# Kernel tuning notes

Measured on AMD Instinct MI355X. Metric: run time of the kernel, lower is better.

## Reference

```python
import jax, jax.numpy as jnp
import numpy as np

SIZE = 5           # kernel size and num_rbfs
MUL = 16           # multiplicity of 0e and 1o in irreps_in/out
CROP = SIZE // 2
# e3nn FullyConnectedTensorProduct path weights (normalization='component', path_normalization='element'):
# path_weight = sqrt((2*l_out+1) / fan_in), fan_in = sum over paths into that output of mul1*mul2.
# out 0e: paths (0e,0e)+(1o,1o) -> fan_in=32; out 1o: paths (0e,1o)+(1o,0e) -> fan_in=32.
PW0 = (1.0 / 32.0) ** 0.5          # scalar output paths
PW1 = (3.0 / 32.0) ** 0.5          # vector output paths
INV_SQRT3 = 3.0 ** -0.5            # wigner-3j values: w3j(1,0,1)=w3j(0,1,1)=w3j(1,1,0)=delta/sqrt(3)


def _lattice_consts():
    # lattice of kernel offsets, steps=(1,1,1) keeps all SIZE points per axis
    r = jnp.linspace(-1.0, 1.0, SIZE)
    lat = jnp.stack(jnp.meshgrid(r, r, r, indexing='ij'), axis=-1)   # [5,5,5,3]
    d = jnp.linalg.norm(lat, axis=-1)                                # [5,5,5]
    # soft_one_hot_linspace(basis='smooth_finite', endpoint=True) over [0,1] with SIZE bins
    values = jnp.linspace(0.0, 1.0, SIZE)
    step = values[1] - values[0]
    diff = (d[..., None] - values) / step                            # [5,5,5,5]
    def sus(t):  # soft unit step: exp(-1/t) for t>0 else 0
        return jnp.where(t > 0, jnp.exp(-1.0 / jnp.where(t > 0, t, 1.0)), 0.0)
    emb = 1.14136 * np.float32(np.e ** 2) * sus(diff + 1.0) * sus(1.0 - diff)
    # spherical harmonics lmax=1, normalize=True, 'component' normalization
    n = lat / jnp.maximum(d, 1e-12)[..., None]                       # zero vector -> 0 (like F.normalize)
    sh0 = jnp.ones_like(d)                                           # l=0 component-normalized
    sh1 = (3.0 ** 0.5) * n                                           # l=1 component-normalized, [5,5,5,3]
    return emb, sh0, sh1


def _make_kernel(weight):
    """emb @ weight -> per-voxel TP weights; tp.right(sh, w) -> [5,5,5,in=64,out=64] kernel."""
    emb, sh0, sh1 = _lattice_consts()
    w = emb @ weight                                                 # [5,5,5,1024]
    S = w.shape[:3]
    blk = MUL * MUL
    # path order: (0e,0e->0e), (0e,1o->1o), (1o,0e->1o), (1o,1o->0e)
    w1, w2, w3, w4 = [w[..., i * blk:(i + 1) * blk].reshape(*S, MUL, MUL) for i in range(4)]
    k_ss = PW0 * w1 * sh0[..., None, None]                           # [s,u,w]   scalar in -> scalar out
    k_sv = PW1 * INV_SQRT3 * jnp.einsum('...uw,...k->...uwk', w2, sh1)   # [s,u,w,k] scalar in -> vector out
    k_vs = PW0 * INV_SQRT3 * jnp.einsum('...uw,...i->...uiw', w4, sh1)   # [s,u,i,w] vector in -> scalar out
    eye3 = jnp.eye(3, dtype=w.dtype)
    k_vv = PW1 * INV_SQRT3 * (w3 * sh0[..., None, None])[..., :, None, :, None] \
           * eye3[None, None, None, None, :, None, :]                # [s,u,i,w,k] vector in -> vector out
    top = jnp.concatenate([k_ss, k_sv.reshape(*S, MUL, 3 * MUL)], axis=-1)            # [s,16,64]
    bot = jnp.concatenate([k_vs.reshape(*S, 3 * MUL, MUL),
                           k_vv.reshape(*S, 3 * MUL, 3 * MUL)], axis=-1)              # [s,48,64]
    kernel = jnp.concatenate([top, bot], axis=-2)                    # [5,5,5,in,out]
    return jnp.transpose(kernel, (4, 3, 0, 1, 2))                    # 'xyzio->oixyz'


def reference(x, weight, w_sc0, w_sc1):
    B = x.shape[0]
    sp = x.shape[2:]
    # self-connection: e3nn Linear (per-irrep mixing, 1/sqrt(fan_in) norm), then crop
    xs = x[:, :MUL]                                                  # scalars [B,16,X,Y,Z]
    xv = x[:, MUL:].reshape(B, MUL, 3, *sp)                          # vectors [B,16,3,X,Y,Z]
    inv = 1.0 / MUL ** 0.5
    sc_s = jnp.einsum('buxyz,uw->bwxyz', xs, w_sc0) * inv
    sc_v = (jnp.einsum('buixyz,uw->bwixyz', xv, w_sc1) * inv).reshape(B, 3 * MUL, *sp)
    sc = jnp.concatenate([sc_s, sc_v], axis=1)[:, :, CROP:-CROP, CROP:-CROP, CROP:-CROP]
    # equivariant kernel + dense conv3d (torch conv3d = correlation = VALID conv here)
    kernel = _make_kernel(weight)                                    # [64,64,5,5,5]
    conv = jax.lax.conv_general_dilated(x, kernel, (1, 1, 1), 'VALID',
                                        dimension_numbers=('NCDHW', 'OIDHW', 'NCDHW'))
    return sc + conv


def setup_inputs() -> dict:
    key = jax.random.key(0)
    k1, k2, k3, k4 = jax.random.split(key, 4)
    weight_numel = 4 * MUL * MUL  # 1024
    return {
        'x': jax.random.normal(k1, (1, 4 * MUL, 56, 56, 56), dtype=jnp.float32),
        'weight': jax.random.normal(k2, (SIZE, weight_numel), dtype=jnp.float32)
                  * np.float32((2.0 / weight_numel) ** 0.5),  # kaiming_normal(relu)
        'w_sc0': jax.random.normal(k3, (MUL, MUL), dtype=jnp.float32),
        'w_sc1': jax.random.normal(k4, (MUL, MUL), dtype=jnp.float32),
    }
```

## Files before the change

kernel.cpp:

```cpp
#include <hip/hip_runtime.h>
#include <hip/hip_bf16.h>

typedef unsigned short ush;
typedef __bf16 v8bf __attribute__((ext_vector_type(8)));
typedef float f32x4 __attribute__((ext_vector_type(4)));
typedef float f32x16 __attribute__((ext_vector_type(16)));

#define SPD 56
#define OSD 52
#define SP3 175616
#define N_A_ELEMS (2*125*64*32)
#define NCX 5488
#define NBA 2008

__global__ void aux_kernel(const float* __restrict__ x, ush* __restrict__ xb,
                           const float* __restrict__ weight, const float* __restrict__ w_sc0,
                           const float* __restrict__ w_sc1, ush* __restrict__ A) {
    __shared__ float t[64 * 33];
    const int bid = blockIdx.x;
    const int tid = threadIdx.x;
    if (bid < NCX) {
        const int s0 = (bid % 2744) * 64;
        const int cg = bid / 2744;
        const int w = tid >> 6, l = tid & 63;
        #pragma unroll
        for (int k = 0; k < 8; k++) {
            int c = w * 8 + k;
            t[l * 33 + c] = x[(cg * 32 + c) * SP3 + s0 + l];
        }
        __syncthreads();
        int v = tid >> 2, qq = tid & 3;
        union { ush u[8]; uint4 q4; } pk;
        #pragma unroll
        for (int j = 0; j < 8; j++) {
            __hip_bfloat16 b = __float2bfloat16(t[v * 33 + qq * 8 + j]);
            pk.u[j] = *(ush*)&b;
        }
        *(uint4*)(xb + ((size_t)(cg * SP3 + s0 + v)) * 32 + qq * 8) = pk.q4;
        return;
    }
    int f = (bid - NCX) * 256 + tid;
    if (f >= N_A_ELEMS) {
        if (f < N_A_ELEMS + 2048) A[f] = 0;
        return;
    }
    int c   = f & 31;
    int o   = (f >> 5) & 63;
    int t2  = f >> 11;
    int tau = t2 % 125;
    int cg  = t2 / 125;
    int i   = cg * 32 + c;
    int dz = tau / 25, dy = (tau / 5) % 5, dx = tau % 5;
    float rz = -1.f + 0.5f * dz, ry = -1.f + 0.5f * dy, rx = -1.f + 0.5f * dx;
    float d = sqrtf(rz * rz + ry * ry + rx * rx);
    float dm = fmaxf(d, 1e-12f);
    float nv[3] = { rz / dm, ry / dm, rx / dm };
    float emb[5];
    #pragma unroll
    for (int m = 0; m < 5; m++) {
        float diff = 4.f * d - (float)m;
        float ta = diff + 1.f, tb = 1.f - diff;
        float sa = ta > 0.f ? expf(-1.f / ta) : 0.f;
        float sb = tb > 0.f ? expf(-1.f / tb) : 0.f;
        emb[m] = 1.14136f * 7.3890560989306495f * sa * sb;
    }
    const float PW0 = 0.17677669529663687f;
    const float PW1 = 0.30618621784789724f;
    const float IS3 = 0.57735026918962576f;
    float val = 0.f;
    int widx = -1; float scale = 0.f;
    if (i < 16) {
        if (o < 16) { widx = i * 16 + o;                         scale = PW0; }
        else        { int wc = (o - 16) / 3, kc = (o - 16) % 3;
                      widx = 256 + i * 16 + wc;                  scale = PW1 * nv[kc]; }
    } else {
        int u = (i - 16) / 3, ic = (i - 16) % 3;
        if (o < 16) { widx = 768 + u * 16 + o;                   scale = PW0 * nv[ic]; }
        else        { int wc = (o - 16) / 3, jc = (o - 16) % 3;
                      if (ic == jc) { widx = 512 + u * 16 + wc;  scale = PW1 * IS3; } }
    }
    if (widx >= 0) {
        float wv = 0.f;
        #pragma unroll
        for (int m = 0; m < 5; m++) wv += emb[m] * weight[m * 1024 + widx];
        val = scale * wv;
    }
    if (tau == 62) {
        if (i < 16 && o < 16) val += 0.25f * w_sc0[i * 16 + o];
        else if (i >= 16 && o >= 16) {
            int u = (i - 16) / 3, ic = (i - 16) % 3;
            int wc = (o - 16) / 3, jc = (o - 16) % 3;
            if (ic == jc) val += 0.25f * w_sc1[u * 16 + wc];
        }
    }
    __hip_bfloat16 b = __float2bfloat16(val);
    A[f] = *(ush*)&b;
}

__launch_bounds__(256, 2)
__global__ void conv_main(const ush* __restrict__ A, const ush* __restrict__ xb,
                          float* __restrict__ out) {
    __shared__ ush patch[32768];

    const int b  = blockIdx.x;
    const int bp = (b & 7) * 148 + (b >> 3);
    if (bp >= 1183) return;
    const int bx = bp % 13;
    const int t1 = bp / 13;
    const int by = t1 % 13;
    const int bz = t1 / 13;
    const int x0 = bx * 4, y0 = by * 4;
    const int z0 = (bz == 6) ? 44 : bz * 8;

    const int tid  = threadIdx.x;
    const int wv   = tid >> 6;
    const int lane = tid & 63;
    const int lhi  = lane >> 5;
    const int rbase32 = ((lane >> 4) & 1) * 64 + ((lane >> 2) & 3) * 8 + (lane & 3);
    const ush* Aw = A + (lane & 31) * 32 + lhi * 8;

    f32x16 acc[2][4];
    #pragma unroll
    for (int mt = 0; mt < 2; mt++)
        #pragma unroll
        for (int nt = 0; nt < 4; nt++)
            acc[mt][nt] = (f32x16)(0.f);

    for (int cg = 0; cg < 2; cg++) {
        __syncthreads();
        #pragma unroll 4
        for (int it = 0; it < 12; it++) {
            int u   = tid + it * 256;
            int qq  = u & 3;
            int vox = u >> 2;
            int xp = vox & 7, yp = (vox >> 3) & 7, zp = vox >> 6;
            const ush* g = xb + ((size_t)((cg * SPD + z0 + zp) * SPD + (y0 + yp)) * SPD + (x0 + xp)) * 32 + qq * 8;
            uint4 v = *(const uint4*)g;
            int slot = vox * 4 + ((qq + vox + (vox >> 3)) & 3);
            *(uint4*)(patch + slot * 8) = v;
        }
        __syncthreads();

        const int t0 = wv * 32;
        int dz = t0 / 25; int rr = t0 - dz * 25; int dy = rr / 5; int dx = rr - dy * 5;

        #pragma unroll 2
        for (int j = 0; j < 32; j++) {
            int t = t0 + j;
            int vb = dz * 64 + dy * 8 + dx;
            if (vb > 292) vb = 0;
            int v0 = vb + rbase32;
            int pre = v0 + (v0 >> 3);
            int slot0 = v0 * 4 + ((lhi + pre) & 3);
            int slot1 = v0 * 4 + ((2 + lhi + pre) & 3);

            v8bf bf[4][2];
            #pragma unroll
            for (int nt = 0; nt < 4; nt++) {
                bf[nt][0] = *(const v8bf*)(patch + slot0 * 8 + nt * 4096);
                bf[nt][1] = *(const v8bf*)(patch + slot1 * 8 + nt * 4096);
            }

            int toff = (t < 125) ? (cg * 125 + t) : 250;
            v8bf af[2][2];
            #pragma unroll
            for (int mt = 0; mt < 2; mt++)
                #pragma unroll
                for (int h = 0; h < 2; h++)
                    af[mt][h] = *(const v8bf*)(Aw + (size_t)toff * 2048 + mt * 1024 + h * 16);

            #pragma unroll
            for (int h = 0; h < 2; h++)
                #pragma unroll
                for (int mt = 0; mt < 2; mt++)
                    #pragma unroll
                    for (int nt = 0; nt < 4; nt++)
                        acc[mt][nt] = __builtin_amdgcn_mfma_f32_32x32x16_bf16(af[mt][h], bf[nt][h], acc[mt][nt], 0, 0, 0);

            int c1 = (dx == 4);
            dx = c1 ? 0 : dx + 1;
            int c2 = c1 & (dy == 4);
            dy = c2 ? 0 : dy + c1;
            dz += c2;
        }
    }

    __syncthreads();
    float* red = (float*)patch;
    if (wv >= 2) {
        #pragma unroll
        for (int mt = 0; mt < 2; mt++)
            #pragma unroll
            for (int nt = 0; nt < 4; nt++) {
                float* p = red + (wv - 2) * 8192 + (mt * 4 + nt) * 1024 + lane * 16;
                #pragma unroll
                for (int s = 0; s < 4; s++) {
                    f32x4 v = { acc[mt][nt][s*4+0], acc[mt][nt][s*4+1], acc[mt][nt][s*4+2], acc[mt][nt][s*4+3] };
                    *(f32x4*)(p + s * 4) = v;
                }
            }
    }
    __syncthreads();
    if (wv < 2) {
        #pragma unroll
        for (int mt = 0; mt < 2; mt++)
            #pragma unroll
            for (int nt = 0; nt < 4; nt++) {
                float* p = red + wv * 8192 + (mt * 4 + nt) * 1024 + lane * 16;
                #pragma unroll
                for (int s = 0; s < 4; s++) {
                    f32x4 v = *(const f32x4*)(p + s * 4);
                    f32x4 m = { acc[mt][nt][s*4+0], acc[mt][nt][s*4+1], acc[mt][nt][s*4+2], acc[mt][nt][s*4+3] };
                    *(f32x4*)(p + s * 4) = v + m;
                }
            }
    }
    __syncthreads();

    const int yy = y0 + ((lane >> 2) & 3);
    const int xx = x0 + (lane & 3);
    #pragma unroll
    for (int k = 0; k < 2; k++) {
        int fi = wv * 2 + k;
        int mt = fi >> 2, nt = fi & 3;
        int zz = z0 + nt * 2 + ((lane >> 4) & 1);
        #pragma unroll
        for (int s = 0; s < 4; s++) {
            f32x4 v = *(const f32x4*)(red + fi * 1024 + lane * 16 + s * 4);
            v += *(const f32x4*)(red + 8192 + fi * 1024 + lane * 16 + s * 4);
            #pragma unroll
            for (int e = 0; e < 4; e++) {
                int o = mt * 32 + e + 8 * s + 4 * lhi;
                out[((o * OSD + zz) * OSD + yy) * OSD + xx] = v[e];
            }
        }
    }
}

extern "C" void kernel_launch(void* const* d_in, const int* in_sizes, int n_in,
                              void* d_out, int out_size, void* d_ws, size_t ws_size,
                              hipStream_t stream) {
    const float* x      = (const float*)d_in[0];
    const float* weight = (const float*)d_in[1];
    const float* w_sc0  = (const float*)d_in[2];
    const float* w_sc1  = (const float*)d_in[3];
    float* out = (float*)d_out;

    ush* A  = (ush*)d_ws;
    ush* xb = (ush*)((char*)d_ws + (2 << 20));

    aux_kernel<<<NCX + NBA, 256, 0, stream>>>(x, xb, weight, w_sc0, w_sc1, A);
    conv_main<<<1184, 256, 0, stream>>>(A, xb, out);
}
```

Before: 231.7 us.

## Split conv waves into 2 N-groups by 2 K-groups and raise occupancy

Each block's four waves are reorganized from four tap-range K-splits into two output-column groups times two tap-range groups. This halves the per-wave accumulator tiles and B-fragment LDS reads, allowing launch bounds of 3 blocks per CU and a smaller shared patch buffer. The cross-wave reduction now uses one exchange and stores output directly, removing a barrier and a pass through LDS. In exchange, each wave loads A fragments for twice as many taps, doubling global/L2 traffic for the weight matrix.

```diff
diff --git a/kernel.cpp b/kernel.cpp
--- a/kernel.cpp
+++ b/kernel.cpp
@@ -97,10 +97,10 @@
     A[f] = *(ush*)&b;
 }
 
-__launch_bounds__(256, 2)
+__launch_bounds__(256, 3)
 __global__ void conv_main(const ush* __restrict__ A, const ush* __restrict__ xb,
                           float* __restrict__ out) {
-    __shared__ ush patch[32768];
+    __shared__ ush patch[24576];
 
     const int b  = blockIdx.x;
     const int bp = (b & 7) * 148 + (b >> 3);
@@ -114,16 +114,18 @@
 
     const int tid  = threadIdx.x;
     const int wv   = tid >> 6;
+    const int ns   = wv & 1;
+    const int ks   = wv >> 1;
     const int lane = tid & 63;
     const int lhi  = lane >> 5;
     const int rbase32 = ((lane >> 4) & 1) * 64 + ((lane >> 2) & 3) * 8 + (lane & 3);
     const ush* Aw = A + (lane & 31) * 32 + lhi * 8;
 
-    f32x16 acc[2][4];
+    f32x16 acc[2][2];
     #pragma unroll
     for (int mt = 0; mt < 2; mt++)
         #pragma unroll
-        for (int nt = 0; nt < 4; nt++)
+        for (int nt = 0; nt < 2; nt++)
             acc[mt][nt] = (f32x16)(0.f);
 
     for (int cg = 0; cg < 2; cg++) {
@@ -141,11 +143,11 @@
         }
         __syncthreads();
 
-        const int t0 = wv * 32;
+        const int t0 = ks * 64;
         int dz = t0 / 25; int rr = t0 - dz * 25; int dy = rr / 5; int dx = rr - dy * 5;
 
         #pragma unroll 2
-        for (int j = 0; j < 32; j++) {
+        for (int j = 0; j < 64; j++) {
             int t = t0 + j;
             int vb = dz * 64 + dy * 8 + dx;
             if (vb > 292) vb = 0;
@@ -154,11 +156,12 @@
             int slot0 = v0 * 4 + ((lhi + pre) & 3);
             int slot1 = v0 * 4 + ((2 + lhi + pre) & 3);
 
-            v8bf bf[4][2];
-            #pragma unroll
-            for (int nt = 0; nt < 4; nt++) {
-                bf[nt][0] = *(const v8bf*)(patch + slot0 * 8 + nt * 4096);
-                bf[nt][1] = *(const v8bf*)(patch + slot1 * 8 + nt * 4096);
+            v8bf bf[2][2];
+            #pragma unroll
+            for (int nt = 0; nt < 2; nt++) {
+                int off = (ns * 2 + nt) * 4096;
+                bf[nt][0] = *(const v8bf*)(patch + slot0 * 8 + off);
+                bf[nt][1] = *(const v8bf*)(patch + slot1 * 8 + off);
             }
 
             int toff = (t < 125) ? (cg * 125 + t) : 250;
@@ -174,7 +177,7 @@
                 #pragma unroll
                 for (int mt = 0; mt < 2; mt++)
                     #pragma unroll
-                    for (int nt = 0; nt < 4; nt++)
+                    for (int nt = 0; nt < 2; nt++)
                         acc[mt][nt] = __builtin_amdgcn_mfma_f32_32x32x16_bf16(af[mt][h], bf[nt][h], acc[mt][nt], 0, 0, 0);
 
             int c1 = (dx == 4);
@@ -187,12 +190,12 @@
 
     __syncthreads();
     float* red = (float*)patch;
-    if (wv >= 2) {
+    if (ks == 1) {
         #pragma unroll
         for (int mt = 0; mt < 2; mt++)
             #pragma unroll
-            for (int nt = 0; nt < 4; nt++) {
-                float* p = red + (wv - 2) * 8192 + (mt * 4 + nt) * 1024 + lane * 16;
+            for (int nt = 0; nt < 2; nt++) {
+                float* p = red + ns * 4096 + (mt * 2 + nt) * 1024 + lane * 16;
                 #pragma unroll
                 for (int s = 0; s < 4; s++) {
                     f32x4 v = { acc[mt][nt][s*4+0], acc[mt][nt][s*4+1], acc[mt][nt][s*4+2], acc[mt][nt][s*4+3] };
@@ -201,39 +204,27 @@
             }
     }
     __syncthreads();
-    if (wv < 2) {
+    if (ks == 0) {
+        const int yy = y0 + ((lane >> 2) & 3);
+        const int xx = x0 + (lane & 3);
         #pragma unroll
         for (int mt = 0; mt < 2; mt++)
             #pragma unroll
-            for (int nt = 0; nt < 4; nt++) {
-                float* p = red + wv * 8192 + (mt * 4 + nt) * 1024 + lane * 16;
+            for (int nt = 0; nt < 2; nt++) {
+                const float* p = red + ns * 4096 + (mt * 2 + nt) * 1024 + lane * 16;
+                int zz = z0 + (ns * 2 + nt) * 2 + ((lane >> 4) & 1);
                 #pragma unroll
                 for (int s = 0; s < 4; s++) {
                     f32x4 v = *(const f32x4*)(p + s * 4);
                     f32x4 m = { acc[mt][nt][s*4+0], acc[mt][nt][s*4+1], acc[mt][nt][s*4+2], acc[mt][nt][s*4+3] };
-                    *(f32x4*)(p + s * 4) = v + m;
+                    v += m;
+                    #pragma unroll
+                    for (int e = 0; e < 4; e++) {
+                        int o = mt * 32 + e + 8 * s + 4 * lhi;
+                        out[((o * OSD + zz) * OSD + yy) * OSD + xx] = v[e];
+                    }
                 }
             }
-    }
-    __syncthreads();
-
-    const int yy = y0 + ((lane >> 2) & 3);
-    const int xx = x0 + (lane & 3);
-    #pragma unroll
-    for (int k = 0; k < 2; k++) {
-        int fi = wv * 2 + k;
-        int mt = fi >> 2, nt = fi & 3;
-        int zz = z0 + nt * 2 + ((lane >> 4) & 1);
-        #pragma unroll
-        for (int s = 0; s < 4; s++) {
-            f32x4 v = *(const f32x4*)(red + fi * 1024 + lane * 16 + s * 4);
-            v += *(const f32x4*)(red + 8192 + fi * 1024 + lane * 16 + s * 4);
-            #pragma unroll
-            for (int e = 0; e < 4; e++) {
-                int o = mt * 32 + e + 8 * s + 4 * lhi;
-                out[((o * OSD + zz) * OSD + yy) * OSD + xx] = v[e];
-            }
-        }
     }
 }
 
```

Result: slower. 263.6 us (+13.7%).
